# Kernel tuning notes

Measured on AMD Instinct MI355X. Metric: run time of the kernel, lower is better.

The kernel has to match this reference:

```python
import jax, jax.numpy as jnp
import numpy as np

N_NODES = 100000
N_EDGES = 1600000
D = 128
N_LAYERS = 3


def _sage_layer(x, src, dst, Wl, Wr, bias, n_nodes):
    # mean aggregation of source-node features at destination nodes
    msg_sum = jax.ops.segment_sum(x[src], dst, num_segments=n_nodes)  # [N, D]
    cnt = jax.ops.segment_sum(jnp.ones((src.shape[0], 1), x.dtype), dst,
                              num_segments=n_nodes)  # [N, 1]
    mean = msg_sum / jnp.maximum(cnt, 1.0)
    # PyG SAGEConv: out = lin_l(aggr) + lin_r(x); lin_l carries the bias
    return mean @ Wl + x @ Wr + bias


def setup_inputs() -> dict:
    key = jax.random.key(0)
    k1, k2, k3, k4, k5 = jax.random.split(key, 5)
    scale = 1.0 / np.sqrt(D)
    x = jax.random.normal(k1, (N_NODES, D), dtype=jnp.float32)
    edge_index = jax.random.randint(k2, (2, N_EDGES), 0, N_NODES, dtype=jnp.int64)
    W_agg = jax.random.normal(k3, (N_LAYERS, D, D), dtype=jnp.float32) * scale
    W_root = jax.random.normal(k4, (N_LAYERS, D, D), dtype=jnp.float32) * scale
    b = jax.random.normal(k5, (N_LAYERS, D), dtype=jnp.float32) * scale
    return {"x": x, "edge_index": edge_index, "W_agg": W_agg,
            "W_root": W_root, "b": b}


def reference(x, edge_index, W_agg, W_root, b):
    src, dst = edge_index[0], edge_index[1]
    n = x.shape[0]
    # hidden layers: conv -> (dropout=identity in eval) -> relu
    for i in range(N_LAYERS - 1):
        x = _sage_layer(x, src, dst, W_agg[i], W_root[i], b[i], n)
        x = jax.nn.relu(x)
    # final layer: no relu
    x = _sage_layer(x, src, dst, W_agg[-1], W_root[-1], b[-1], n)
    return x
```

## Files before the change

kernel.cpp:

```cpp
#include <hip/hip_runtime.h>
#include <stdint.h>

#define D 128
#define CHUNK 3200

typedef __attribute__((ext_vector_type(8))) __bf16 bf16x8;
typedef __attribute__((ext_vector_type(4))) __bf16 bf16x4;
typedef __attribute__((ext_vector_type(4))) float f32x4;

__global__ void detect_idx(const void* ei, int* flag, int n_nodes) {
    if (blockIdx.x == 0 && threadIdx.x == 0) {
        const long long* p = (const long long*)ei;
        int is64 = 1;
        for (int i = 0; i < 64; ++i) {
            long long v = p[i];
            if (v < 0 || v >= (long long)n_nodes) { is64 = 0; break; }
        }
        *flag = is64;
    }
}

__global__ void convert_idx(const void* ei, const int* flag,
                            int* src32, int* dst32, int nE) {
    int e = blockIdx.x * blockDim.x + threadIdx.x;
    if (e >= nE) return;
    if (*flag) {
        const long long* p = (const long long*)ei;
        src32[e] = (int)p[e];
        dst32[e] = (int)p[(size_t)nE + e];
    } else {
        const int* p = (const int*)ei;
        src32[e] = p[e];
        dst32[e] = p[nE + e];
    }
}

__global__ __launch_bounds__(256) void bucket_hist(
        const int* __restrict__ dst32, int* __restrict__ bcnt, int nE) {
    __shared__ int l[256];
    l[threadIdx.x] = 0;
    __syncthreads();
    int stride = gridDim.x * 256;
    for (int e = blockIdx.x * 256 + threadIdx.x; e < nE; e += stride)
        atomicAdd(&l[dst32[e] >> 9], 1);
    __syncthreads();
    int v = l[threadIdx.x];
    if (v) atomicAdd(&bcnt[threadIdx.x], v);
}

__global__ void bucket_scan(const int* __restrict__ bcnt, int* __restrict__ bstart,
                            int* __restrict__ bcur, int G, int nE,
                            int* __restrict__ offsets, int n) {
    __shared__ int s[256];
    int t = threadIdx.x;
    int v = (t < G) ? bcnt[t] : 0;
    s[t] = v;
    __syncthreads();
    for (int off = 1; off < 256; off <<= 1) {
        int u = 0;
        if (t >= off) u = s[t - off];
        __syncthreads();
        if (t >= off) s[t] += u;
        __syncthreads();
    }
    if (t < G) { int ex = s[t] - v; bstart[t] = ex; bcur[t] = ex; }
    if (t == 0) offsets[n] = nE;
}

__global__ __launch_bounds__(256) void bucket_fill(
        const int* __restrict__ src32, const int* __restrict__ dst32,
        int* __restrict__ bcur, int* __restrict__ ebs, int* __restrict__ ebd,
        int nE) {
    __shared__ int ls[CHUNK], ld_[CHUNK];
    __shared__ int lcnt[256], lbase[256], lcur[256];
    int e0 = blockIdx.x * CHUNK;
    int cnt = nE - e0;
    if (cnt > CHUNK) cnt = CHUNK;
    if (cnt < 0) cnt = 0;
    for (int i = threadIdx.x; i < cnt; i += 256) {
        ls[i]  = src32[e0 + i];
        ld_[i] = dst32[e0 + i];
    }
    lcnt[threadIdx.x] = 0;
    __syncthreads();
    for (int i = threadIdx.x; i < cnt; i += 256)
        atomicAdd(&lcnt[ld_[i] >> 9], 1);
    __syncthreads();
    int c = lcnt[threadIdx.x];
    if (c > 0) lbase[threadIdx.x] = atomicAdd(&bcur[threadIdx.x], c);
    lcur[threadIdx.x] = 0;
    __syncthreads();
    for (int i = threadIdx.x; i < cnt; i += 256) {
        int g = ld_[i] >> 9;
        int p = lbase[g] + atomicAdd(&lcur[g], 1);
        ebs[p] = ls[i];
        ebd[p] = ld_[i];
    }
}

__global__ __launch_bounds__(256) void bucket_scatter(
        const int* __restrict__ ebs, const int* __restrict__ ebd,
        const int* __restrict__ bstart, const int* __restrict__ bcnt,
        int* __restrict__ offsets, int* __restrict__ csr, int n) {
    __shared__ int ncnt[512], nofs[512], ps[256];
    int g = blockIdx.x;
    int base = bstart[g];
    int cnt = bcnt[g];
    int n0 = g << 9;
    int nr = n - n0; if (nr > 512) nr = 512;
    for (int i = threadIdx.x; i < 512; i += 256) ncnt[i] = 0;
    __syncthreads();
    for (int i = threadIdx.x; i < cnt; i += 256)
        atomicAdd(&ncnt[ebd[base + i] - n0], 1);
    __syncthreads();
    int t = threadIdx.x;
    int c0 = ncnt[2 * t], c1 = ncnt[2 * t + 1];
    ps[t] = c0 + c1;
    __syncthreads();
    for (int off = 1; off < 256; off <<= 1) {
        int u = 0;
        if (t >= off) u = ps[t - off];
        __syncthreads();
        if (t >= off) ps[t] += u;
        __syncthreads();
    }
    int pex = ps[t] - (c0 + c1);
    nofs[2 * t] = pex;
    nofs[2 * t + 1] = pex + c0;
    __syncthreads();
    for (int i = threadIdx.x; i < nr; i += 256)
        offsets[n0 + i] = base + nofs[i];
    for (int i = threadIdx.x; i < 512; i += 256) ncnt[i] = 0;
    __syncthreads();
    for (int i = threadIdx.x; i < cnt; i += 256) {
        int d = ebd[base + i] - n0;
        int p = base + nofs[d] + atomicAdd(&ncnt[d], 1);
        csr[p] = ebs[base + i];
    }
}

__global__ void build_wt(const float* __restrict__ Wa, const float* __restrict__ Wr,
                         __bf16* __restrict__ WtHi, __bf16* __restrict__ WtLo) {
    int idx = blockIdx.x * 256 + threadIdx.x;
    if (idx >= 3 * 128 * 256) return;
    int L = idx / (128 * 256);
    int rem = idx % (128 * 256);
    int c = rem / 256;
    int k = rem % 256;
    float v = (k < 128) ? Wa[((size_t)L * 128 + k) * 128 + c]
                        : Wr[((size_t)L * 128 + (k - 128)) * 128 + c];
    __bf16 h = (__bf16)v;
    __bf16 l = (__bf16)(v - (float)h);
    WtHi[idx] = h;
    WtLo[idx] = l;
}

__global__ void cvt_x(const float* __restrict__ x, __bf16* __restrict__ a,
                      int total8) {
    int i = blockIdx.x * 256 + threadIdx.x;
    if (i >= total8) return;
    const float4* p = (const float4*)(x + (size_t)i * 8);
    float4 v0 = p[0], v1 = p[1];
    float vv[8] = {v0.x, v0.y, v0.z, v0.w, v1.x, v1.y, v1.z, v1.w};
    bf16x8 h;
    #pragma unroll
    for (int j = 0; j < 8; ++j) h[j] = (__bf16)vv[j];
    *(bf16x8*)(a + (size_t)i * 8) = h;
}

__global__ __launch_bounds__(256) void agg_mean5(
        const __bf16* __restrict__ act, const int* __restrict__ csr,
        const int* __restrict__ offs, __bf16* __restrict__ mean, int n) {
    int node = (blockIdx.x * blockDim.x + threadIdx.x) >> 4;
    int l8 = (threadIdx.x & 15) << 3;
    if (node >= n) return;
    int beg = offs[node], end = offs[node + 1];
    float acc[8] = {0.f, 0.f, 0.f, 0.f, 0.f, 0.f, 0.f, 0.f};
    int i = beg;
    for (; i + 8 <= end; i += 8) {
        bf16x8 v[8];
        #pragma unroll
        for (int u = 0; u < 8; ++u)
            v[u] = *(const bf16x8*)(act + (size_t)csr[i + u] * D + l8);
        #pragma unroll
        for (int u = 0; u < 8; ++u)
            #pragma unroll
            for (int j = 0; j < 8; ++j) acc[j] += (float)v[u][j];
    }
    for (; i + 4 <= end; i += 4) {
        bf16x8 v[4];
        #pragma unroll
        for (int u = 0; u < 4; ++u)
            v[u] = *(const bf16x8*)(act + (size_t)csr[i + u] * D + l8);
        #pragma unroll
        for (int u = 0; u < 4; ++u)
            #pragma unroll
            for (int j = 0; j < 8; ++j) acc[j] += (float)v[u][j];
    }
    for (; i < end; ++i) {
        bf16x8 v = *(const bf16x8*)(act + (size_t)csr[i] * D + l8);
        #pragma unroll
        for (int j = 0; j < 8; ++j) acc[j] += (float)v[j];
    }
    int deg = end - beg;
    float inv = 1.0f / (float)(deg > 1 ? deg : 1);
    bf16x8 h;
    #pragma unroll
    for (int j = 0; j < 8; ++j) h[j] = (__bf16)(acc[j] * inv);
    *(bf16x8*)(mean + (size_t)node * D + l8) = h;
}

__global__ __launch_bounds__(512, 4) void sage_gemm7(
        const __bf16* __restrict__ mean, const __bf16* __restrict__ act,
        const __bf16* __restrict__ WtHi, const __bf16* __restrict__ WtLo,
        const float* __restrict__ bias,
        __bf16* __restrict__ oB, float* __restrict__ oF,
        int n, int mode, int ntiles) {
    __shared__ __align__(16) char sA[2][8192];
    __shared__ __align__(16) char sC[8192];
    int tid  = threadIdx.x;
    int wave = tid >> 6;
    int lane = tid & 63;
    int r16  = lane & 15;
    int kg   = lane >> 4;
    int colbase = wave * 16;

    bf16x8 BH[8], BL[8];
    #pragma unroll
    for (int c8 = 0; c8 < 8; ++c8) {
        size_t o = (size_t)(colbase + r16) * 256 + c8 * 32 + kg * 8;
        BH[c8] = *(const bf16x8*)(WtHi + o);
        BL[c8] = *(const bf16x8*)(WtLo + o);
    }
    float4 bv = *(const float4*)(bias + colbase + kg * 4);

    int xm = (r16 & 7) << 4;
    int kb[8];
    #pragma unroll
    for (int c8 = 0; c8 < 8; ++c8)
        kb[c8] = r16 * 512 + ((c8 * 64 + kg * 16) ^ xm);

    int srow = tid >> 5;
    int sc16 = tid & 31;
    int sdst = srow * 512 + ((sc16 * 16) ^ ((srow & 7) << 4));

    auto stage_load = [&](int t, int4& r) {
        int grow = t * 16 + srow;
        if (grow < n) {
            const __bf16* src = (sc16 < 16)
                ? (mean + (size_t)grow * D + sc16 * 8)
                : (act  + (size_t)grow * D + (sc16 - 16) * 8);
            r = *(const int4*)src;
        } else {
            r = make_int4(0, 0, 0, 0);
        }
    };

    int tstride = gridDim.x;
    int t = blockIdx.x;

    int4 sreg = make_int4(0, 0, 0, 0);
    if (t < ntiles) stage_load(t, sreg);
    *(int4*)(sA[0] + sdst) = sreg;
    __syncthreads();
    int cur = 0;

    for (; t < ntiles; t += tstride) {
        int tn = t + tstride;
        bool hasnext = tn < ntiles;
        int4 nreg;
        if (hasnext) stage_load(tn, nreg);

        f32x4 acc = (f32x4){0.f, 0.f, 0.f, 0.f};
        const char* base = sA[cur];
        #pragma unroll
        for (int c8 = 0; c8 < 8; ++c8) {
            bf16x8 a = *(const bf16x8*)(base + kb[c8]);
            acc = __builtin_amdgcn_mfma_f32_16x16x32_bf16(BH[c8], a, acc, 0, 0, 0);
            acc = __builtin_amdgcn_mfma_f32_16x16x32_bf16(BL[c8], a, acc, 0, 0, 0);
        }

        __syncthreads();
        if (hasnext) *(int4*)(sA[cur ^ 1] + sdst) = nreg;

        float v0 = acc[0] + bv.x;
        float v1 = acc[1] + bv.y;
        float v2 = acc[2] + bv.z;
        float v3 = acc[3] + bv.w;
        if (mode == 0) {
            v0 = fmaxf(v0, 0.f); v1 = fmaxf(v1, 0.f);
            v2 = fmaxf(v2, 0.f); v3 = fmaxf(v3, 0.f);
            bf16x4 h4;
            h4[0] = (__bf16)v0; h4[1] = (__bf16)v1;
            h4[2] = (__bf16)v2; h4[3] = (__bf16)v3;
            *(bf16x4*)(sC + r16 * 256 + (colbase + kg * 4) * 2) = h4;
        } else {
            *(f32x4*)(sC + r16 * 512 + (colbase + kg * 4) * 4) =
                (f32x4){v0, v1, v2, v3};
        }
        __syncthreads();

        if (mode == 0) {
            if (tid < 256) {
                int rr = tid >> 4, c16 = tid & 15;
                int grow = t * 16 + rr;
                if (grow < n) {
                    int4 h = *(const int4*)(sC + rr * 256 + c16 * 16);
                    *(int4*)(oB + (size_t)grow * D + c16 * 8) = h;
                }
            }
        } else {
            int rr = tid >> 5, c = tid & 31;
            int grow = t * 16 + rr;
            if (grow < n) {
                f32x4 f = *(const f32x4*)(sC + rr * 512 + c * 16);
                *(f32x4*)(oF + (size_t)grow * D + c * 4) = f;
            }
        }
        cur ^= 1;
    }
}

extern "C" void kernel_launch(void* const* d_in, const int* in_sizes, int n_in,
                              void* d_out, int out_size, void* d_ws, size_t ws_size,
                              hipStream_t stream) {
    const float* x  = (const float*)d_in[0];
    const void*  ei = d_in[1];
    const float* Wa = (const float*)d_in[2];
    const float* Wr = (const float*)d_in[3];
    const float* bb = (const float*)d_in[4];
    float* outp = (float*)d_out;

    int n  = in_sizes[0] / D;
    int nE = in_sizes[1] / 2;
    int G  = (n + 511) >> 9;

    char* ws = (char*)d_ws;
    size_t off = 0;
    auto alloc = [&](size_t bytes) -> char* {
        char* p = ws + off;
        off = (off + bytes + 255) & ~(size_t)255;
        return p;
    };
    int* flag      = (int*)alloc(4);
    int* src32     = (int*)alloc((size_t)nE * 4);
    int* dst32     = (int*)alloc((size_t)nE * 4);
    int* offsets   = (int*)alloc(((size_t)n + 1) * 4);
    int* csr_src   = (int*)alloc((size_t)nE * 4);
    int* ebs       = (int*)alloc((size_t)nE * 4);
    int* ebd       = (int*)alloc((size_t)nE * 4);
    int* bcnt      = (int*)alloc(1024);
    int* bstart    = (int*)alloc(1024);
    int* bcur      = (int*)alloc(1024);
    __bf16* actA   = (__bf16*)alloc((size_t)n * D * 2);
    __bf16* actB   = (__bf16*)alloc((size_t)n * D * 2);
    __bf16* meanP  = (__bf16*)alloc((size_t)n * D * 2);
    __bf16* WtHi   = (__bf16*)alloc((size_t)3 * 128 * 256 * 2);
    __bf16* WtLo   = (__bf16*)alloc((size_t)3 * 128 * 256 * 2);
    (void)ws_size; (void)n_in; (void)out_size;

    const int B = 256;
    int ge = (nE + B - 1) / B;

    hipLaunchKernelGGL(detect_idx, dim3(1), dim3(64), 0, stream, ei, flag, n);
    hipLaunchKernelGGL(convert_idx, dim3(ge), dim3(B), 0, stream,
                       ei, flag, src32, dst32, nE);
    hipLaunchKernelGGL(build_wt, dim3(384), dim3(256), 0, stream, Wa, Wr, WtHi, WtLo);
    int total8 = n * D / 8;
    hipLaunchKernelGGL(cvt_x, dim3((total8 + 255) / 256), dim3(256), 0, stream,
                       x, actA, total8);

    hipMemsetAsync(bcnt, 0, 1024, stream);
    hipLaunchKernelGGL(bucket_hist, dim3(512), dim3(B), 0, stream, dst32, bcnt, nE);
    hipLaunchKernelGGL(bucket_scan, dim3(1), dim3(B), 0, stream,
                       bcnt, bstart, bcur, G, nE, offsets, n);
    hipLaunchKernelGGL(bucket_fill, dim3((nE + CHUNK - 1) / CHUNK), dim3(B), 0, stream,
                       src32, dst32, bcur, ebs, ebd, nE);
    hipLaunchKernelGGL(bucket_scatter, dim3(G), dim3(B), 0, stream,
                       ebs, ebd, bstart, bcnt, offsets, csr_src, n);

    int agg_blocks = (n * 16 + B - 1) / B;
    int ntiles = (n + 15) / 16;
    int gemm_grid = 512;
    const int WSTRIDE = 128 * 256;

    hipLaunchKernelGGL(agg_mean5, dim3(agg_blocks), dim3(B), 0, stream,
                       actA, csr_src, offsets, meanP, n);
    hipLaunchKernelGGL(sage_gemm7, dim3(gemm_grid), dim3(512), 0, stream,
                       meanP, actA, WtHi + 0 * WSTRIDE, WtLo + 0 * WSTRIDE,
                       bb + 0 * D, actB, outp, n, 0, ntiles);

    hipLaunchKernelGGL(agg_mean5, dim3(agg_blocks), dim3(B), 0, stream,
                       actB, csr_src, offsets, meanP, n);
    hipLaunchKernelGGL(sage_gemm7, dim3(gemm_grid), dim3(512), 0, stream,
                       meanP, actB, WtHi + 1 * WSTRIDE, WtLo + 1 * WSTRIDE,
                       bb + 1 * D, actA, outp, n, 0, ntiles);

    hipLaunchKernelGGL(agg_mean5, dim3(agg_blocks), dim3(B), 0, stream,
                       actA, csr_src, offsets, meanP, n);
    hipLaunchKernelGGL(sage_gemm7, dim3(gemm_grid), dim3(512), 0, stream,
                       meanP, actA, WtHi + 2 * WSTRIDE, WtLo + 2 * WSTRIDE,
                       bb + 2 * D, actB, outp, n, 1, ntiles);
}
```

Baseline: 349.4 us.

## Fuse mean aggregation into the SAGE GEMM kernel per 16-row tile

Merges the gather-mean aggregation kernel into the GEMM kernel. Each 512-thread block aggregates neighbour rows for its 16-node tile, splitting each node's edge list across two half-groups and combining the partial sums through shared memory. The mean and root features then go straight into the LDS A tile for the MFMA. This removes the write and re-read of the intermediate mean buffer and one launch per layer. In exchange it gives up the double-buffered prefetch, adds more barriers per tile, and restricts the gather to 512 persistent blocks, which may lower memory-level parallelism for the latency-bound gathers.

```diff
diff --git a/kernel.cpp b/kernel.cpp
--- a/kernel.cpp
+++ b/kernel.cpp
@@ -168,56 +168,15 @@
     *(bf16x8*)(a + (size_t)i * 8) = h;
 }
 
-__global__ __launch_bounds__(256) void agg_mean5(
+__global__ __launch_bounds__(512, 4) void sage_fused(
         const __bf16* __restrict__ act, const int* __restrict__ csr,
-        const int* __restrict__ offs, __bf16* __restrict__ mean, int n) {
-    int node = (blockIdx.x * blockDim.x + threadIdx.x) >> 4;
-    int l8 = (threadIdx.x & 15) << 3;
-    if (node >= n) return;
-    int beg = offs[node], end = offs[node + 1];
-    float acc[8] = {0.f, 0.f, 0.f, 0.f, 0.f, 0.f, 0.f, 0.f};
-    int i = beg;
-    for (; i + 8 <= end; i += 8) {
-        bf16x8 v[8];
-        #pragma unroll
-        for (int u = 0; u < 8; ++u)
-            v[u] = *(const bf16x8*)(act + (size_t)csr[i + u] * D + l8);
-        #pragma unroll
-        for (int u = 0; u < 8; ++u)
-            #pragma unroll
-            for (int j = 0; j < 8; ++j) acc[j] += (float)v[u][j];
-    }
-    for (; i + 4 <= end; i += 4) {
-        bf16x8 v[4];
-        #pragma unroll
-        for (int u = 0; u < 4; ++u)
-            v[u] = *(const bf16x8*)(act + (size_t)csr[i + u] * D + l8);
-        #pragma unroll
-        for (int u = 0; u < 4; ++u)
-            #pragma unroll
-            for (int j = 0; j < 8; ++j) acc[j] += (float)v[u][j];
-    }
-    for (; i < end; ++i) {
-        bf16x8 v = *(const bf16x8*)(act + (size_t)csr[i] * D + l8);
-        #pragma unroll
-        for (int j = 0; j < 8; ++j) acc[j] += (float)v[j];
-    }
-    int deg = end - beg;
-    float inv = 1.0f / (float)(deg > 1 ? deg : 1);
-    bf16x8 h;
-    #pragma unroll
-    for (int j = 0; j < 8; ++j) h[j] = (__bf16)(acc[j] * inv);
-    *(bf16x8*)(mean + (size_t)node * D + l8) = h;
-}
-
-__global__ __launch_bounds__(512, 4) void sage_gemm7(
-        const __bf16* __restrict__ mean, const __bf16* __restrict__ act,
+        const int* __restrict__ offs,
         const __bf16* __restrict__ WtHi, const __bf16* __restrict__ WtLo,
         const float* __restrict__ bias,
         __bf16* __restrict__ oB, float* __restrict__ oF,
         int n, int mode, int ntiles) {
-    __shared__ __align__(16) char sA[2][8192];
-    __shared__ __align__(16) char sC[8192];
+    __shared__ __align__(16) char sA[8192];
+    __shared__ __align__(16) char sU[8192];
     int tid  = threadIdx.x;
     int wave = tid >> 6;
     int lane = tid & 63;
@@ -240,48 +199,76 @@
     for (int c8 = 0; c8 < 8; ++c8)
         kb[c8] = r16 * 512 + ((c8 * 64 + kg * 16) ^ xm);
 
-    int srow = tid >> 5;
-    int sc16 = tid & 31;
-    int sdst = srow * 512 + ((sc16 * 16) ^ ((srow & 7) << 4));
-
-    auto stage_load = [&](int t, int4& r) {
-        int grow = t * 16 + srow;
-        if (grow < n) {
-            const __bf16* src = (sc16 < 16)
-                ? (mean + (size_t)grow * D + sc16 * 8)
-                : (act  + (size_t)grow * D + (sc16 - 16) * 8);
-            r = *(const int4*)src;
-        } else {
-            r = make_int4(0, 0, 0, 0);
-        }
-    };
-
-    int tstride = gridDim.x;
-    int t = blockIdx.x;
-
-    int4 sreg = make_int4(0, 0, 0, 0);
-    if (t < ntiles) stage_load(t, sreg);
-    *(int4*)(sA[0] + sdst) = sreg;
-    __syncthreads();
-    int cur = 0;
-
-    for (; t < ntiles; t += tstride) {
-        int tn = t + tstride;
-        bool hasnext = tn < ntiles;
-        int4 nreg;
-        if (hasnext) stage_load(tn, nreg);
+    int g    = tid >> 4;
+    int l16  = tid & 15;
+    int lrow = g & 15;
+    bool hiH = g >= 16;
+
+    for (int t = blockIdx.x; t < ntiles; t += gridDim.x) {
+        int r = t * 16 + lrow;
+
+        float a0=0.f,a1=0.f,a2=0.f,a3=0.f,a4=0.f,a5=0.f,a6=0.f,a7=0.f;
+        int beg = 0, end = 0;
+        if (r < n) { beg = offs[r]; end = offs[r + 1]; }
+        int deg = end - beg;
+        int mid = beg + ((deg + 1) >> 1);
+        int lo = hiH ? mid : beg;
+        int hi = hiH ? end : mid;
+        int i = lo;
+        for (; i + 8 <= hi; i += 8) {
+            bf16x8 v[8];
+            #pragma unroll
+            for (int u = 0; u < 8; ++u)
+                v[u] = *(const bf16x8*)(act + (size_t)csr[i + u] * D + l16 * 8);
+            #pragma unroll
+            for (int u = 0; u < 8; ++u) {
+                a0 += (float)v[u][0]; a1 += (float)v[u][1];
+                a2 += (float)v[u][2]; a3 += (float)v[u][3];
+                a4 += (float)v[u][4]; a5 += (float)v[u][5];
+                a6 += (float)v[u][6]; a7 += (float)v[u][7];
+            }
+        }
+        for (; i < hi; ++i) {
+            bf16x8 v = *(const bf16x8*)(act + (size_t)csr[i] * D + l16 * 8);
+            a0 += (float)v[0]; a1 += (float)v[1];
+            a2 += (float)v[2]; a3 += (float)v[3];
+            a4 += (float)v[4]; a5 += (float)v[5];
+            a6 += (float)v[6]; a7 += (float)v[7];
+        }
+
+        if (hiH) {
+            float* sp = (float*)sU + ((lrow << 4) + l16) * 8;
+            sp[0]=a0; sp[1]=a1; sp[2]=a2; sp[3]=a3;
+            sp[4]=a4; sp[5]=a5; sp[6]=a6; sp[7]=a7;
+            int4 av = make_int4(0, 0, 0, 0);
+            if (r < n) av = *(const int4*)(act + (size_t)r * D + l16 * 8);
+            *(int4*)(sA + lrow * 512 + ((((16 + l16) * 16)) ^ ((lrow & 7) << 4))) = av;
+        }
+        __syncthreads();
+
+        if (!hiH) {
+            const float* sp = (const float*)sU + ((lrow << 4) + l16) * 8;
+            float inv = 1.0f / (float)(deg > 1 ? deg : 1);
+            bf16x8 m;
+            m[0] = (__bf16)((a0 + sp[0]) * inv);
+            m[1] = (__bf16)((a1 + sp[1]) * inv);
+            m[2] = (__bf16)((a2 + sp[2]) * inv);
+            m[3] = (__bf16)((a3 + sp[3]) * inv);
+            m[4] = (__bf16)((a4 + sp[4]) * inv);
+            m[5] = (__bf16)((a5 + sp[5]) * inv);
+            m[6] = (__bf16)((a6 + sp[6]) * inv);
+            m[7] = (__bf16)((a7 + sp[7]) * inv);
+            *(bf16x8*)(sA + lrow * 512 + ((l16 * 16) ^ ((lrow & 7) << 4))) = m;
+        }
+        __syncthreads();
 
         f32x4 acc = (f32x4){0.f, 0.f, 0.f, 0.f};
-        const char* base = sA[cur];
         #pragma unroll
         for (int c8 = 0; c8 < 8; ++c8) {
-            bf16x8 a = *(const bf16x8*)(base + kb[c8]);
+            bf16x8 a = *(const bf16x8*)(sA + kb[c8]);
             acc = __builtin_amdgcn_mfma_f32_16x16x32_bf16(BH[c8], a, acc, 0, 0, 0);
             acc = __builtin_amdgcn_mfma_f32_16x16x32_bf16(BL[c8], a, acc, 0, 0, 0);
         }
-
-        __syncthreads();
-        if (hasnext) *(int4*)(sA[cur ^ 1] + sdst) = nreg;
 
         float v0 = acc[0] + bv.x;
         float v1 = acc[1] + bv.y;
@@ -293,9 +280,9 @@
             bf16x4 h4;
             h4[0] = (__bf16)v0; h4[1] = (__bf16)v1;
             h4[2] = (__bf16)v2; h4[3] = (__bf16)v3;
-            *(bf16x4*)(sC + r16 * 256 + (colbase + kg * 4) * 2) = h4;
+            *(bf16x4*)(sU + r16 * 256 + (colbase + kg * 4) * 2) = h4;
         } else {
-            *(f32x4*)(sC + r16 * 512 + (colbase + kg * 4) * 4) =
+            *(f32x4*)(sU + r16 * 512 + (colbase + kg * 4) * 4) =
                 (f32x4){v0, v1, v2, v3};
         }
         __syncthreads();
@@ -305,7 +292,7 @@
                 int rr = tid >> 4, c16 = tid & 15;
                 int grow = t * 16 + rr;
                 if (grow < n) {
-                    int4 h = *(const int4*)(sC + rr * 256 + c16 * 16);
+                    int4 h = *(const int4*)(sU + rr * 256 + c16 * 16);
                     *(int4*)(oB + (size_t)grow * D + c16 * 8) = h;
                 }
             }
@@ -313,11 +300,11 @@
             int rr = tid >> 5, c = tid & 31;
             int grow = t * 16 + rr;
             if (grow < n) {
-                f32x4 f = *(const f32x4*)(sC + rr * 512 + c * 16);
+                f32x4 f = *(const f32x4*)(sU + rr * 512 + c * 16);
                 *(f32x4*)(oF + (size_t)grow * D + c * 4) = f;
             }
         }
-        cur ^= 1;
+        __syncthreads();
     }
 }
 
@@ -354,7 +341,6 @@
     int* bcur      = (int*)alloc(1024);
     __bf16* actA   = (__bf16*)alloc((size_t)n * D * 2);
     __bf16* actB   = (__bf16*)alloc((size_t)n * D * 2);
-    __bf16* meanP  = (__bf16*)alloc((size_t)n * D * 2);
     __bf16* WtHi   = (__bf16*)alloc((size_t)3 * 128 * 256 * 2);
     __bf16* WtLo   = (__bf16*)alloc((size_t)3 * 128 * 256 * 2);
     (void)ws_size; (void)n_in; (void)out_size;
@@ -379,26 +365,19 @@
     hipLaunchKernelGGL(bucket_scatter, dim3(G), dim3(B), 0, stream,
                        ebs, ebd, bstart, bcnt, offsets, csr_src, n);
 
-    int agg_blocks = (n * 16 + B - 1) / B;
     int ntiles = (n + 15) / 16;
-    int gemm_grid = 512;
+    int grid = 512;
     const int WSTRIDE = 128 * 256;
 
-    hipLaunchKernelGGL(agg_mean5, dim3(agg_blocks), dim3(B), 0, stream,
-                       actA, csr_src, offsets, meanP, n);
-    hipLaunchKernelGGL(sage_gemm7, dim3(gemm_grid), dim3(512), 0, stream,
-                       meanP, actA, WtHi + 0 * WSTRIDE, WtLo + 0 * WSTRIDE,
+    hipLaunchKernelGGL(sage_fused, dim3(grid), dim3(512), 0, stream,
+                       actA, csr_src, offsets, WtHi + 0 * WSTRIDE, WtLo + 0 * WSTRIDE,
                        bb + 0 * D, actB, outp, n, 0, ntiles);
 
-    hipLaunchKernelGGL(agg_mean5, dim3(agg_blocks), dim3(B), 0, stream,
-                       actB, csr_src, offsets, meanP, n);
-    hipLaunchKernelGGL(sage_gemm7, dim3(gemm_grid), dim3(512), 0, stream,
-                       meanP, actB, WtHi + 1 * WSTRIDE, WtLo + 1 * WSTRIDE,
+    hipLaunchKernelGGL(sage_fused, dim3(grid), dim3(512), 0, stream,
+                       actB, csr_src, offsets, WtHi + 1 * WSTRIDE, WtLo + 1 * WSTRIDE,
                        bb + 1 * D, actA, outp, n, 0, ntiles);
 
-    hipLaunchKernelGGL(agg_mean5, dim3(agg_blocks), dim3(B), 0, stream,
-                       actA, csr_src, offsets, meanP, n);
-    hipLaunchKernelGGL(sage_gemm7, dim3(gemm_grid), dim3(512), 0, stream,
-                       meanP, actA, WtHi + 2 * WSTRIDE, WtLo + 2 * WSTRIDE,
+    hipLaunchKernelGGL(sage_fused, dim3(grid), dim3(512), 0, stream,
+                       actA, csr_src, offsets, WtHi + 2 * WSTRIDE, WtLo + 2 * WSTRIDE,
                        bb + 2 * D, actB, outp, n, 1, ntiles);
 }
```

Result: slower. 466.6 us (+33.5%).

## Fuse index conversion with histogram and pack edges into 32-bit words

Applied to the files above, without the earlier changes.

Index conversion and bucket histogram now run as one kernel that packs each edge into a single 32-bit word (source shifted by 9, low 9 bits of destination) plus a one-byte bucket id. Bucket fill and scatter move one word per edge instead of two ints, which cuts traffic through the CSR build. CHUNK is doubled and the GEMM grid is doubled. The packing assumes source ids fit in 23 bits and at most 256 buckets, which holds for this graph size.

```diff
diff --git a/kernel.cpp b/kernel.cpp
--- a/kernel.cpp
+++ b/kernel.cpp
@@ -2,7 +2,7 @@
 #include <stdint.h>
 
 #define D 128
-#define CHUNK 3200
+#define CHUNK 6400
 
 typedef __attribute__((ext_vector_type(8))) __bf16 bf16x8;
 typedef __attribute__((ext_vector_type(4))) __bf16 bf16x4;
@@ -20,29 +20,30 @@
     }
 }
 
-__global__ void convert_idx(const void* ei, const int* flag,
-                            int* src32, int* dst32, int nE) {
-    int e = blockIdx.x * blockDim.x + threadIdx.x;
-    if (e >= nE) return;
-    if (*flag) {
-        const long long* p = (const long long*)ei;
-        src32[e] = (int)p[e];
-        dst32[e] = (int)p[(size_t)nE + e];
-    } else {
-        const int* p = (const int*)ei;
-        src32[e] = p[e];
-        dst32[e] = p[nE + e];
-    }
-}
-
-__global__ __launch_bounds__(256) void bucket_hist(
-        const int* __restrict__ dst32, int* __restrict__ bcnt, int nE) {
+__global__ __launch_bounds__(256) void convert_pack(
+        const void* __restrict__ ei, const int* __restrict__ flag,
+        unsigned int* __restrict__ eword, unsigned char* __restrict__ gb,
+        int* __restrict__ bcnt, int nE) {
     __shared__ int l[256];
     l[threadIdx.x] = 0;
     __syncthreads();
+    bool is64 = *flag != 0;
     int stride = gridDim.x * 256;
-    for (int e = blockIdx.x * 256 + threadIdx.x; e < nE; e += stride)
-        atomicAdd(&l[dst32[e] >> 9], 1);
+    for (int e = blockIdx.x * 256 + threadIdx.x; e < nE; e += stride) {
+        int s, d;
+        if (is64) {
+            const long long* p = (const long long*)ei;
+            s = (int)p[e];
+            d = (int)p[(size_t)nE + e];
+        } else {
+            const int* p = (const int*)ei;
+            s = p[e];
+            d = p[nE + e];
+        }
+        eword[e] = ((unsigned)s << 9) | (unsigned)(d & 511);
+        gb[e] = (unsigned char)(d >> 9);
+        atomicAdd(&l[d >> 9], 1);
+    }
     __syncthreads();
     int v = l[threadIdx.x];
     if (v) atomicAdd(&bcnt[threadIdx.x], v);
@@ -67,39 +68,38 @@
     if (t == 0) offsets[n] = nE;
 }
 
-__global__ __launch_bounds__(256) void bucket_fill(
-        const int* __restrict__ src32, const int* __restrict__ dst32,
-        int* __restrict__ bcur, int* __restrict__ ebs, int* __restrict__ ebd,
-        int nE) {
-    __shared__ int ls[CHUNK], ld_[CHUNK];
+__global__ __launch_bounds__(256) void bucket_fill2(
+        const unsigned int* __restrict__ eword, const unsigned char* __restrict__ gb,
+        int* __restrict__ bcur, unsigned int* __restrict__ ebuf, int nE) {
+    __shared__ unsigned int lw[CHUNK];
+    __shared__ unsigned char lg[CHUNK];
     __shared__ int lcnt[256], lbase[256], lcur[256];
     int e0 = blockIdx.x * CHUNK;
     int cnt = nE - e0;
     if (cnt > CHUNK) cnt = CHUNK;
     if (cnt < 0) cnt = 0;
     for (int i = threadIdx.x; i < cnt; i += 256) {
-        ls[i]  = src32[e0 + i];
-        ld_[i] = dst32[e0 + i];
+        lw[i] = eword[e0 + i];
+        lg[i] = gb[e0 + i];
     }
     lcnt[threadIdx.x] = 0;
     __syncthreads();
     for (int i = threadIdx.x; i < cnt; i += 256)
-        atomicAdd(&lcnt[ld_[i] >> 9], 1);
+        atomicAdd(&lcnt[lg[i]], 1);
     __syncthreads();
     int c = lcnt[threadIdx.x];
     if (c > 0) lbase[threadIdx.x] = atomicAdd(&bcur[threadIdx.x], c);
     lcur[threadIdx.x] = 0;
     __syncthreads();
     for (int i = threadIdx.x; i < cnt; i += 256) {
-        int g = ld_[i] >> 9;
+        int g = lg[i];
         int p = lbase[g] + atomicAdd(&lcur[g], 1);
-        ebs[p] = ls[i];
-        ebd[p] = ld_[i];
-    }
-}
-
-__global__ __launch_bounds__(256) void bucket_scatter(
-        const int* __restrict__ ebs, const int* __restrict__ ebd,
+        ebuf[p] = lw[i];
+    }
+}
+
+__global__ __launch_bounds__(256) void bucket_scatter2(
+        const unsigned int* __restrict__ ebuf,
         const int* __restrict__ bstart, const int* __restrict__ bcnt,
         int* __restrict__ offsets, int* __restrict__ csr, int n) {
     __shared__ int ncnt[512], nofs[512], ps[256];
@@ -111,7 +111,7 @@
     for (int i = threadIdx.x; i < 512; i += 256) ncnt[i] = 0;
     __syncthreads();
     for (int i = threadIdx.x; i < cnt; i += 256)
-        atomicAdd(&ncnt[ebd[base + i] - n0], 1);
+        atomicAdd(&ncnt[ebuf[base + i] & 511], 1);
     __syncthreads();
     int t = threadIdx.x;
     int c0 = ncnt[2 * t], c1 = ncnt[2 * t + 1];
@@ -133,9 +133,10 @@
     for (int i = threadIdx.x; i < 512; i += 256) ncnt[i] = 0;
     __syncthreads();
     for (int i = threadIdx.x; i < cnt; i += 256) {
-        int d = ebd[base + i] - n0;
+        unsigned int w = ebuf[base + i];
+        int d = w & 511;
         int p = base + nofs[d] + atomicAdd(&ncnt[d], 1);
-        csr[p] = ebs[base + i];
+        csr[p] = (int)(w >> 9);
     }
 }
 
@@ -342,46 +343,43 @@
         off = (off + bytes + 255) & ~(size_t)255;
         return p;
     };
-    int* flag      = (int*)alloc(4);
-    int* src32     = (int*)alloc((size_t)nE * 4);
-    int* dst32     = (int*)alloc((size_t)nE * 4);
-    int* offsets   = (int*)alloc(((size_t)n + 1) * 4);
-    int* csr_src   = (int*)alloc((size_t)nE * 4);
-    int* ebs       = (int*)alloc((size_t)nE * 4);
-    int* ebd       = (int*)alloc((size_t)nE * 4);
-    int* bcnt      = (int*)alloc(1024);
-    int* bstart    = (int*)alloc(1024);
-    int* bcur      = (int*)alloc(1024);
-    __bf16* actA   = (__bf16*)alloc((size_t)n * D * 2);
-    __bf16* actB   = (__bf16*)alloc((size_t)n * D * 2);
-    __bf16* meanP  = (__bf16*)alloc((size_t)n * D * 2);
-    __bf16* WtHi   = (__bf16*)alloc((size_t)3 * 128 * 256 * 2);
-    __bf16* WtLo   = (__bf16*)alloc((size_t)3 * 128 * 256 * 2);
+    int* flag            = (int*)alloc(4);
+    unsigned int* eword  = (unsigned int*)alloc((size_t)nE * 4);
+    unsigned char* gbuf  = (unsigned char*)alloc((size_t)nE);
+    unsigned int* ebuf   = (unsigned int*)alloc((size_t)nE * 4);
+    int* offsets         = (int*)alloc(((size_t)n + 1) * 4);
+    int* csr_src         = (int*)alloc((size_t)nE * 4);
+    int* bcnt            = (int*)alloc(1024);
+    int* bstart          = (int*)alloc(1024);
+    int* bcur            = (int*)alloc(1024);
+    __bf16* actA         = (__bf16*)alloc((size_t)n * D * 2);
+    __bf16* actB         = (__bf16*)alloc((size_t)n * D * 2);
+    __bf16* meanP        = (__bf16*)alloc((size_t)n * D * 2);
+    __bf16* WtHi         = (__bf16*)alloc((size_t)3 * 128 * 256 * 2);
+    __bf16* WtLo         = (__bf16*)alloc((size_t)3 * 128 * 256 * 2);
     (void)ws_size; (void)n_in; (void)out_size;
 
     const int B = 256;
-    int ge = (nE + B - 1) / B;
 
     hipLaunchKernelGGL(detect_idx, dim3(1), dim3(64), 0, stream, ei, flag, n);
-    hipLaunchKernelGGL(convert_idx, dim3(ge), dim3(B), 0, stream,
-                       ei, flag, src32, dst32, nE);
+    hipMemsetAsync(bcnt, 0, 1024, stream);
+    hipLaunchKernelGGL(convert_pack, dim3(512), dim3(B), 0, stream,
+                       ei, flag, eword, gbuf, bcnt, nE);
     hipLaunchKernelGGL(build_wt, dim3(384), dim3(256), 0, stream, Wa, Wr, WtHi, WtLo);
     int total8 = n * D / 8;
     hipLaunchKernelGGL(cvt_x, dim3((total8 + 255) / 256), dim3(256), 0, stream,
                        x, actA, total8);
 
-    hipMemsetAsync(bcnt, 0, 1024, stream);
-    hipLaunchKernelGGL(bucket_hist, dim3(512), dim3(B), 0, stream, dst32, bcnt, nE);
     hipLaunchKernelGGL(bucket_scan, dim3(1), dim3(B), 0, stream,
                        bcnt, bstart, bcur, G, nE, offsets, n);
-    hipLaunchKernelGGL(bucket_fill, dim3((nE + CHUNK - 1) / CHUNK), dim3(B), 0, stream,
-                       src32, dst32, bcur, ebs, ebd, nE);
-    hipLaunchKernelGGL(bucket_scatter, dim3(G), dim3(B), 0, stream,
-                       ebs, ebd, bstart, bcnt, offsets, csr_src, n);
+    hipLaunchKernelGGL(bucket_fill2, dim3((nE + CHUNK - 1) / CHUNK), dim3(B), 0, stream,
+                       eword, gbuf, bcur, ebuf, nE);
+    hipLaunchKernelGGL(bucket_scatter2, dim3(G), dim3(B), 0, stream,
+                       ebuf, bstart, bcnt, offsets, csr_src, n);
 
     int agg_blocks = (n * 16 + B - 1) / B;
     int ntiles = (n + 15) / 16;
-    int gemm_grid = 512;
+    int gemm_grid = 1024;
     const int WSTRIDE = 128 * 256;
 
     hipLaunchKernelGGL(agg_mean5, dim3(agg_blocks), dim3(B), 0, stream,
```

After: 343.9 us. About the same (-1.6%).
